# Kernel optimization log

Measured on AMD Instinct MI355X. Metric: run time of the kernel, lower is better.

The kernel has to match this reference:

```python
import jax, jax.numpy as jnp
import numpy as np

N_NODES = 50000
N_EDGES = 800000
NFEAT, NHID, NOUT = 128, 128, 64


def _glorot(key, shape):
    lim = 1.0 / np.sqrt(shape[0])
    return jax.random.uniform(key, shape, jnp.float32, -lim, lim)


def setup_inputs() -> dict:
    key = jax.random.key(0)
    ks = jax.random.split(key, 12)
    x = jax.random.normal(ks[0], (N_NODES, NFEAT), jnp.float32)
    edge_src = jax.random.randint(ks[1], (N_EDGES,), 0, N_NODES, jnp.int32)
    edge_dst = jax.random.randint(ks[2], (N_EDGES,), 0, N_NODES, jnp.int32)
    edge_w = jax.random.uniform(ks[3], (N_EDGES,), jnp.float32)  # normalized adj values
    # layer params: nfeat->nhid, nhid->nhid, nhid->nhid, nhid->nout
    W0, b0 = _glorot(ks[4], (NFEAT, NHID)), jnp.zeros((NHID,), jnp.float32)
    W1, b1 = _glorot(ks[5], (NHID, NHID)), jnp.zeros((NHID,), jnp.float32)
    W2, b2 = _glorot(ks[6], (NHID, NHID)), jnp.zeros((NHID,), jnp.float32)
    W3, b3 = _glorot(ks[7], (NHID, NOUT)), jnp.zeros((NOUT,), jnp.float32)
    return dict(x=x, edge_src=edge_src, edge_dst=edge_dst, edge_w=edge_w,
                W0=W0, b0=b0, W1=W1, b1=b1, W2=W2, b2=b2, W3=W3, b3=b3)


def _gcn_layer(h, src, dst, w, W, b):
    # support = h @ W ; out = A @ support + b  (A given as weighted edge list)
    support = h @ W                               # [N, d_out]
    msgs = support[src] * w[:, None]              # [E, d_out] gather + scale
    agg = jax.ops.segment_sum(msgs, dst, num_segments=N_NODES)  # scatter-add
    return agg + b


def reference(x, edge_src, edge_dst, edge_w, W0, b0, W1, b1, W2, b2, W3, b3):
    # eval mode: dropout is identity
    h = jax.nn.relu(_gcn_layer(x, edge_src, edge_dst, edge_w, W0, b0))
    h = jax.nn.relu(_gcn_layer(h, edge_src, edge_dst, edge_w, W1, b1))
    h = jax.nn.relu(_gcn_layer(h, edge_src, edge_dst, edge_w, W2, b2))
    h = _gcn_layer(h, edge_src, edge_dst, edge_w, W3, b3)  # no relu on last layer
    return h
```

## Files before the change

kernel.cpp:

```cpp
#include <hip/hip_runtime.h>


constexpr int NN = 50000;
constexpr int NE = 800000;
constexpr int NB = (NN + 127) >> 7;
constexpr int CAP = 4608;
constexpr int PART_CHUNK = 4096;
constexpr int PART_GRID = (NE + PART_CHUNK - 1) / PART_CHUNK;

typedef __attribute__((ext_vector_type(8))) short bf16x8;
typedef __attribute__((ext_vector_type(4))) float floatx4;
typedef __attribute__((ext_vector_type(2))) float floatx2;
typedef __attribute__((ext_vector_type(4))) unsigned int uintx4;
typedef __attribute__((ext_vector_type(2))) unsigned int uintx2;

__device__ inline unsigned short f2bf(float f) {
    unsigned u = __float_as_uint(f);
    u += 0x7fffu + ((u >> 16) & 1u);
    return (unsigned short)(u >> 16);
}
__device__ inline float bflo(unsigned v) { return __uint_as_float(v << 16); }
__device__ inline float bfhi(unsigned v) { return __uint_as_float(v & 0xffff0000u); }
__device__ inline unsigned char f2fp8(float f) {
    return (unsigned char)(__builtin_amdgcn_cvt_pk_fp8_f32(f, f, 0, false) & 0xff);
}


__global__ __launch_bounds__(256) void k_part(
        const int* __restrict__ src, const int* __restrict__ dst,
        const float* __restrict__ w, int* __restrict__ bfill,
        int2* __restrict__ ep) {
    __shared__ int hist[NB], base[NB], off[NB];
    int tid = threadIdx.x;
    for (int b = tid; b < NB; b += 256) { hist[b] = 0; off[b] = 0; }
    __syncthreads();

    int e0 = blockIdx.x * PART_CHUNK;
    int  sreg[16]; int wreg[16]; short breg[16];
#pragma unroll
    for (int i = 0; i < 16; ++i) {
        int e = e0 + i * 256 + tid;
        if (e < NE) {
            int d = dst[e];
            int b = d >> 7;
            sreg[i] = (src[e] & 0xffff) | ((d & 127) << 16);
            wreg[i] = __float_as_int(w[e]);
            breg[i] = (short)b;
            atomicAdd(&hist[b], 1);
        } else breg[i] = -1;
    }
    __syncthreads();
    for (int b = tid; b < NB; b += 256)
        base[b] = b * CAP + atomicAdd(&bfill[b], hist[b]);
    __syncthreads();
#pragma unroll
    for (int i = 0; i < 16; ++i) {
        if (breg[i] >= 0) {
            int b = breg[i];
            int p = atomicAdd(&off[b], 1);
            ep[base[b] + p] = make_int2(sreg[i], wreg[i]);
        }
    }
}

__global__ __launch_bounds__(256) void k_sort(
        const int2* __restrict__ ep, const int* __restrict__ bfill,
        unsigned* __restrict__ es, int2* __restrict__ begend) {
    __shared__ int cnt[128], base[128], fl[128];
    __shared__ int s_total;
    int b  = blockIdx.x;
    int n0 = b << 7;
    int nn = min(128, NN - n0);
    int t  = threadIdx.x;
    if (t < 128) { cnt[t] = 0; fl[t] = 0; }
    __syncthreads();
    int bbase = b * CAP;
    int beg = bbase, end = bbase + bfill[b];
    for (int e = beg + t; e < end; e += 256)
        atomicAdd(&cnt[(ep[e].x >> 16) & 127], 1);
    __syncthreads();
    int cp = (t < 128) ? ((cnt[t] + 3) & ~3) : 0;
    if (t < 128) base[t] = cp;
    __syncthreads();
    for (int off = 1; off < 128; off <<= 1) {
        int add = (t >= off && t < 128) ? base[t - off] : 0;
        __syncthreads();
        if (t < 128) base[t] += add;
        __syncthreads();
    }
    if (t == 127) s_total = base[127];
    __syncthreads();
    int total = s_total;
    for (int i = t; i < total + 16; i += 256) es[bbase + i] = 0u;
    if (t < nn) {
        int off = base[t] - cp;
        begend[n0 + t] = make_int2(bbase + off, bbase + off + cp);
    }
    __syncthreads();
    for (int e = beg + t; e < end; e += 256) {
        int2 v = ep[e];
        int d = (v.x >> 16) & 127;
        int off = base[d] - ((cnt[d] + 3) & ~3);
        int pos = bbase + off + atomicAdd(&fl[d], 1);
        es[pos] = (unsigned)(v.x & 0xffff) |
                  ((unsigned)f2bf(__int_as_float(v.y)) << 16);
    }
}


__global__ void k_prep(
        const float* __restrict__ W0, const float* __restrict__ W1,
        const float* __restrict__ W2, const float* __restrict__ W3,
        unsigned short* __restrict__ T0, unsigned short* __restrict__ T1,
        unsigned short* __restrict__ T2, unsigned short* __restrict__ T3,
        int* __restrict__ bfill) {
    int b = blockIdx.x;
    if (b == 448) {
        for (int i = threadIdx.x; i < NB; i += 128) bfill[i] = 0;
        return;
    }
    const float* W; unsigned short* T; int N, n;
    if (b < 128)      { W = W0; T = T0; N = 128; n = b; }
    else if (b < 256) { W = W1; T = T1; N = 128; n = b - 128; }
    else if (b < 384) { W = W2; T = T2; N = 128; n = b - 256; }
    else              { W = W3; T = T3; N = 64;  n = b - 384; }
    int k = threadIdx.x;
    T[n * 128 + k] = f2bf(W[(size_t)k * N + n]);
}


__device__ inline bf16x8 ldA_f32(const float* A, size_t off) {
    float4 u = *(const float4*)&A[off];
    float4 v = *(const float4*)&A[off + 4];
    bf16x8 r;
    r[0] = (short)f2bf(u.x); r[1] = (short)f2bf(u.y);
    r[2] = (short)f2bf(u.z); r[3] = (short)f2bf(u.w);
    r[4] = (short)f2bf(v.x); r[5] = (short)f2bf(v.y);
    r[6] = (short)f2bf(v.z); r[7] = (short)f2bf(v.w);
    return r;
}

__global__ __launch_bounds__(256) void k_gemm0(
        const float* __restrict__ A,
        const unsigned short* __restrict__ Wt,
        unsigned char* __restrict__ C,
        int M) {
    constexpr int STR = 136;
    __shared__ unsigned short sWt[128 * STR];

    const int tid = threadIdx.x;
#pragma unroll
    for (int i = 0; i < 8; ++i) {
        int c = i * 256 + tid;
        int row = c >> 4, col = (c & 15) * 8;
        *(uint4*)&sWt[row * STR + col] = *(const uint4*)&Wt[row * 128 + col];
    }

    const int wv = tid >> 6;
    const int ln = tid & 63;
    const int m  = ln & 15;
    const int qd = ln >> 4;

    int gr  = blockIdx.x * 64 + wv * 16 + m;
    int grc = (gr < M) ? gr : (M - 1);
    bf16x8 af[4];
#pragma unroll
    for (int s = 0; s < 4; ++s)
        af[s] = ldA_f32(A, (size_t)grc * 128 + s * 32 + qd * 8);

    __syncthreads();

    floatx4 acc[8];
#pragma unroll
    for (int c = 0; c < 8; ++c) {
        acc[c] = (floatx4){0.f, 0.f, 0.f, 0.f};
#pragma unroll
        for (int s = 0; s < 4; ++s) {
            bf16x8 bf = *(const bf16x8*)&sWt[(c * 16 + m) * STR + s * 32 + qd * 8];
            acc[c] = __builtin_amdgcn_mfma_f32_16x16x32_bf16(af[s], bf, acc[c], 0, 0, 0);
        }
    }

    int row0 = blockIdx.x * 64 + wv * 16 + qd * 4;
#pragma unroll
    for (int c = 0; c < 8; ++c)
#pragma unroll
        for (int r = 0; r < 4; ++r) {
            int row = row0 + r;
            if (row < M) {
                int col = c * 16 + m;
                int sl  = col >> 6;
                C[(size_t)sl * NN * 64 + (size_t)row * 64 + (col & 63)] =
                    f2fp8(acc[c][r]);
            }
        }
}


template<int NO, typename CT>
__global__ __launch_bounds__(256) void k_gemmh(
        const unsigned short* __restrict__ A,
        const unsigned short* __restrict__ Wt,
        CT* __restrict__ C,
        int M) {
    constexpr int STR = 136;
    __shared__ unsigned short sWt[NO * STR];

    const int tid = threadIdx.x;
#pragma unroll
    for (int i = 0; i < NO / 16; ++i) {
        int c = i * 256 + tid;
        int row = c >> 4, col = (c & 15) * 8;
        *(uint4*)&sWt[row * STR + col] = *(const uint4*)&Wt[row * 128 + col];
    }

    const int wv = tid >> 6;
    const int ln = tid & 63;
    const int m  = ln & 15;
    const int qd = ln >> 4;

    int gr  = blockIdx.x * 64 + wv * 16 + m;
    int grc = (gr < M) ? gr : (M - 1);
    bf16x8 af[4];
#pragma unroll
    for (int s = 0; s < 4; ++s)
        af[s] = __builtin_nontemporal_load(
            (const bf16x8*)&A[(size_t)grc * 128 + s * 32 + qd * 8]);

    __syncthreads();

    floatx4 acc[NO / 16];
#pragma unroll
    for (int c = 0; c < NO / 16; ++c) {
        acc[c] = (floatx4){0.f, 0.f, 0.f, 0.f};
#pragma unroll
        for (int s = 0; s < 4; ++s) {
            bf16x8 bf = *(const bf16x8*)&sWt[(c * 16 + m) * STR + s * 32 + qd * 8];
            acc[c] = __builtin_amdgcn_mfma_f32_16x16x32_bf16(af[s], bf, acc[c], 0, 0, 0);
        }
    }

    int row0 = blockIdx.x * 64 + wv * 16 + qd * 4;
#pragma unroll
    for (int c = 0; c < NO / 16; ++c)
#pragma unroll
        for (int r = 0; r < 4; ++r) {
            int row = row0 + r;
            if (row < M) {
                int col = c * 16 + m;
                if constexpr (sizeof(CT) == 1) {
                    int sl = col >> 6;
                    C[(size_t)sl * NN * 64 + (size_t)row * 64 + (col & 63)] =
                        (CT)f2fp8(acc[c][r]);
                } else {
                    int sl = col >> 5;
                    C[(size_t)sl * NN * 32 + (size_t)row * 32 + (col & 31)] =
                        (CT)f2bf(acc[c][r]);
                }
            }
        }
}


#define FMAP8(W, R)                                                             \
    { floatx2 p0 = __builtin_amdgcn_cvt_pk_f32_fp8((int)(R).x, false);          \
      floatx2 p1 = __builtin_amdgcn_cvt_pk_f32_fp8((int)(R).x, true);           \
      floatx2 p2 = __builtin_amdgcn_cvt_pk_f32_fp8((int)(R).y, false);          \
      floatx2 p3 = __builtin_amdgcn_cvt_pk_f32_fp8((int)(R).y, true);           \
      acc[0] = fmaf(W, p0.x, acc[0]); acc[1] = fmaf(W, p0.y, acc[1]);           \
      acc[2] = fmaf(W, p1.x, acc[2]); acc[3] = fmaf(W, p1.y, acc[3]);           \
      acc[4] = fmaf(W, p2.x, acc[4]); acc[5] = fmaf(W, p2.y, acc[5]);           \
      acc[6] = fmaf(W, p3.x, acc[6]); acc[7] = fmaf(W, p3.y, acc[7]); }

__global__ __launch_bounds__(256, 8) void k_aggh(
        const unsigned char* __restrict__ sup,
        const int2* __restrict__ begend, const unsigned* __restrict__ es,
        const float* __restrict__ bias,
        unsigned short* __restrict__ h) {
    const int bid  = blockIdx.x;
    const int sl   = bid & 1;
    const int tile = bid >> 1;
    const int tid  = threadIdx.x;
    const int l    = tid & 7;
    const int n    = tile * 32 + (tid >> 3);
    const bool nv  = n < NN;
    const unsigned char* supS = sup + (size_t)sl * NN * 64;
    const float* biasS = bias + sl * 64;

    int2 be = nv ? begend[n] : make_int2(0, 0);
    const int e0 = be.x, en = be.y;
    int e = e0;
    float acc[8] = {0.f, 0.f, 0.f, 0.f, 0.f, 0.f, 0.f, 0.f};
    bool v = e < en;
    if (__any(v)) {
        uintx4 mv = __builtin_nontemporal_load((const uintx4*)&es[e0]);
        for (;;) {
            uint2 r0 = *(const uint2*)&supS[(size_t)(mv[0] & 0xffffu) * 64 + l * 8];
            uint2 r1 = *(const uint2*)&supS[(size_t)(mv[1] & 0xffffu) * 64 + l * 8];
            uint2 r2 = *(const uint2*)&supS[(size_t)(mv[2] & 0xffffu) * 64 + l * 8];
            uint2 r3 = *(const uint2*)&supS[(size_t)(mv[3] & 0xffffu) * 64 + l * 8];
            float w0 = v ? bfhi(mv[0]) : 0.f;
            float w1 = v ? bfhi(mv[1]) : 0.f;
            float w2 = v ? bfhi(mv[2]) : 0.f;
            float w3 = v ? bfhi(mv[3]) : 0.f;
            e += 4;
            v = e < en;
            bool more = __any(v);
            int eo = v ? e : e0;
            uintx4 mn = __builtin_nontemporal_load((const uintx4*)&es[eo]);
            FMAP8(w0, r0); FMAP8(w1, r1); FMAP8(w2, r2); FMAP8(w3, r3);
            mv = mn;
            if (!more) break;
        }
    }
    if (nv) {
        uintx4 pk;
#pragma unroll
        for (int q = 0; q < 4; ++q) {
            float a0 = fmaxf(acc[2 * q]     + biasS[l * 8 + 2 * q],     0.f);
            float a1 = fmaxf(acc[2 * q + 1] + biasS[l * 8 + 2 * q + 1], 0.f);
            pk[q] = (unsigned)f2bf(a0) | ((unsigned)f2bf(a1) << 16);
        }
        __builtin_nontemporal_store(
            pk, (uintx4*)&h[(size_t)n * 128 + sl * 64 + l * 8]);
    }
}


#define FMA4(W, R)                                                              \
    acc[0] = fmaf(W, bflo((R).x), acc[0]); acc[1] = fmaf(W, bfhi((R).x), acc[1]); \
    acc[2] = fmaf(W, bflo((R).y), acc[2]); acc[3] = fmaf(W, bfhi((R).y), acc[3]);

__global__ __launch_bounds__(256, 8) void k_aggo(
        const unsigned short* __restrict__ sup,
        const int2* __restrict__ begend, const unsigned* __restrict__ es,
        const float* __restrict__ bias, float* __restrict__ out) {
    const int bid  = blockIdx.x;
    const int sl   = bid & 1;
    const int tile = bid >> 1;
    const int tid  = threadIdx.x;
    const int l    = tid & 7;
    const int n    = tile * 32 + (tid >> 3);
    const bool nv  = n < NN;
    const unsigned short* supS = sup + (size_t)sl * NN * 32;
    const float* biasS = bias + sl * 32;

    int2 be = nv ? begend[n] : make_int2(0, 0);
    const int e0 = be.x, en = be.y;
    int e = e0;
    float acc[4] = {0.f, 0.f, 0.f, 0.f};
    bool v = e < en;
    if (__any(v)) {
        uintx4 mv = __builtin_nontemporal_load((const uintx4*)&es[e0]);
        for (;;) {
            uint2 r0 = *(const uint2*)&supS[(size_t)(mv[0] & 0xffffu) * 32 + l * 4];
            uint2 r1 = *(const uint2*)&supS[(size_t)(mv[1] & 0xffffu) * 32 + l * 4];
            uint2 r2 = *(const uint2*)&supS[(size_t)(mv[2] & 0xffffu) * 32 + l * 4];
            uint2 r3 = *(const uint2*)&supS[(size_t)(mv[3] & 0xffffu) * 32 + l * 4];
            float w0 = v ? bfhi(mv[0]) : 0.f;
            float w1 = v ? bfhi(mv[1]) : 0.f;
            float w2 = v ? bfhi(mv[2]) : 0.f;
            float w3 = v ? bfhi(mv[3]) : 0.f;
            e += 4;
            v = e < en;
            bool more = __any(v);
            int eo = v ? e : e0;
            uintx4 mn = __builtin_nontemporal_load((const uintx4*)&es[eo]);
            FMA4(w0, r0); FMA4(w1, r1); FMA4(w2, r2); FMA4(w3, r3);
            mv = mn;
            if (!more) break;
        }
    }
    if (nv) {
        float4 o = make_float4(acc[0] + biasS[l * 4],
                               acc[1] + biasS[l * 4 + 1],
                               acc[2] + biasS[l * 4 + 2],
                               acc[3] + biasS[l * 4 + 3]);
        *(float4*)&out[(size_t)n * 64 + sl * 32 + l * 4] = o;
    }
}


extern "C" void kernel_launch(void* const* d_in, const int* in_sizes, int n_in,
                              void* d_out, int out_size, void* d_ws, size_t ws_size,
                              hipStream_t stream) {
    (void)in_sizes; (void)n_in; (void)out_size; (void)ws_size;

    const float* x    = (const float*)d_in[0];
    const int*   esrc = (const int*)d_in[1];
    const int*   edst = (const int*)d_in[2];
    const float* ew   = (const float*)d_in[3];
    const float* W0   = (const float*)d_in[4];
    const float* b0   = (const float*)d_in[5];
    const float* W1   = (const float*)d_in[6];
    const float* b1   = (const float*)d_in[7];
    const float* W2   = (const float*)d_in[8];
    const float* b2   = (const float*)d_in[9];
    const float* W3   = (const float*)d_in[10];
    const float* b3   = (const float*)d_in[11];

    char* p = (char*)d_ws;
    auto alloc = [&](size_t bytes) {
        char* r = p;
        p += (bytes + 511) & ~size_t(511);
        return r;
    };
    int*      bfill  = (int*)     alloc((size_t)NB * 4);
    int2*     begend = (int2*)    alloc((size_t)NN * 8);
    int2*     ep     = (int2*)    alloc((size_t)NB * CAP * 8);
    unsigned* es     = (unsigned*)alloc((size_t)NB * CAP * 4);
    unsigned char*  s8a  = (unsigned char*) alloc((size_t)NN * 128);
    unsigned char*  s8b  = (unsigned char*) alloc((size_t)NN * 128);
    unsigned short* s16  = (unsigned short*)alloc((size_t)NN * 64 * 2);
    unsigned short* hbuf = (unsigned short*)alloc((size_t)NN * 128 * 2);
    unsigned short* Wt0 = (unsigned short*)alloc((size_t)128 * 128 * 2);
    unsigned short* Wt1 = (unsigned short*)alloc((size_t)128 * 128 * 2);
    unsigned short* Wt2 = (unsigned short*)alloc((size_t)128 * 128 * 2);
    unsigned short* Wt3 = (unsigned short*)alloc((size_t)64 * 128 * 2);

    k_prep<<<449, 128, 0, stream>>>(W0, W1, W2, W3, Wt0, Wt1, Wt2, Wt3, bfill);
    k_part<<<PART_GRID, 256, 0, stream>>>(esrc, edst, ew, bfill, ep);
    k_sort<<<NB, 256, 0, stream>>>(ep, bfill, es, begend);

    const int g_gemm = (NN + 63) / 64;
    const int g_agg  = ((NN + 31) / 32) * 2;

    k_gemm0<<<g_gemm, 256, 0, stream>>>(x, Wt0, s8a, NN);
    k_aggh<<<g_agg, 256, 0, stream>>>(s8a, begend, es, b0, hbuf);
    k_gemmh<128, unsigned char><<<g_gemm, 256, 0, stream>>>(hbuf, Wt1, s8b, NN);
    k_aggh<<<g_agg, 256, 0, stream>>>(s8b, begend, es, b1, hbuf);
    k_gemmh<128, unsigned char><<<g_gemm, 256, 0, stream>>>(hbuf, Wt2, s8a, NN);
    k_aggh<<<g_agg, 256, 0, stream>>>(s8a, begend, es, b2, hbuf);
    k_gemmh<64, unsigned short><<<g_gemm, 256, 0, stream>>>(hbuf, Wt3, s16, NN);
    k_aggo<<<g_agg, 256, 0, stream>>>(s16, begend, es, b3, (float*)d_out);
}
```

Baseline: 253.3 us.

## Build CSR with global per-node histogram, scan, and atomic scatter; unroll aggregation by eight

Replaces the two-pass bucketed partition and sort with a per-node histogram, a block scan that claims segments from a global cursor, and a direct atomic scatter into a compact CSR edge array. Each node's segment is padded to a multiple of eight, and the aggregation kernels now load eight edges per iteration instead of four, so more gather loads are in flight. In exchange the build uses global atomics on 50k counters and a scatter whose order within a segment is nondeterministic. Padding to eight also adds more zero-weight padding entries that the aggregation still reads.

```diff
diff --git a/kernel.cpp b/kernel.cpp
--- a/kernel.cpp
+++ b/kernel.cpp
@@ -4,15 +4,12 @@
 constexpr int NN = 50000;
 constexpr int NE = 800000;
 constexpr int NB = (NN + 127) >> 7;
-constexpr int CAP = 4608;
-constexpr int PART_CHUNK = 4096;
-constexpr int PART_GRID = (NE + PART_CHUNK - 1) / PART_CHUNK;
+constexpr int ES_CAP = NE + 7 * NN + 64;
 
 typedef __attribute__((ext_vector_type(8))) short bf16x8;
 typedef __attribute__((ext_vector_type(4))) float floatx4;
 typedef __attribute__((ext_vector_type(2))) float floatx2;
 typedef __attribute__((ext_vector_type(4))) unsigned int uintx4;
-typedef __attribute__((ext_vector_type(2))) unsigned int uintx2;
 
 __device__ inline unsigned short f2bf(float f) {
     unsigned u = __float_as_uint(f);
@@ -26,84 +23,68 @@
 }
 
 
-__global__ __launch_bounds__(256) void k_part(
-        const int* __restrict__ src, const int* __restrict__ dst,
-        const float* __restrict__ w, int* __restrict__ bfill,
-        int2* __restrict__ ep) {
-    __shared__ int hist[NB], base[NB], off[NB];
-    int tid = threadIdx.x;
-    for (int b = tid; b < NB; b += 256) { hist[b] = 0; off[b] = 0; }
-    __syncthreads();
-
-    int e0 = blockIdx.x * PART_CHUNK;
-    int  sreg[16]; int wreg[16]; short breg[16];
-#pragma unroll
-    for (int i = 0; i < 16; ++i) {
-        int e = e0 + i * 256 + tid;
-        if (e < NE) {
-            int d = dst[e];
-            int b = d >> 7;
-            sreg[i] = (src[e] & 0xffff) | ((d & 127) << 16);
-            wreg[i] = __float_as_int(w[e]);
-            breg[i] = (short)b;
-            atomicAdd(&hist[b], 1);
-        } else breg[i] = -1;
-    }
-    __syncthreads();
-    for (int b = tid; b < NB; b += 256)
-        base[b] = b * CAP + atomicAdd(&bfill[b], hist[b]);
-    __syncthreads();
-#pragma unroll
-    for (int i = 0; i < 16; ++i) {
-        if (breg[i] >= 0) {
-            int b = breg[i];
-            int p = atomicAdd(&off[b], 1);
-            ep[base[b] + p] = make_int2(sreg[i], wreg[i]);
-        }
-    }
-}
-
-__global__ __launch_bounds__(256) void k_sort(
-        const int2* __restrict__ ep, const int* __restrict__ bfill,
-        unsigned* __restrict__ es, int2* __restrict__ begend) {
-    __shared__ int cnt[128], base[128], fl[128];
-    __shared__ int s_total;
-    int b  = blockIdx.x;
-    int n0 = b << 7;
-    int nn = min(128, NN - n0);
-    int t  = threadIdx.x;
-    if (t < 128) { cnt[t] = 0; fl[t] = 0; }
-    __syncthreads();
-    int bbase = b * CAP;
-    int beg = bbase, end = bbase + bfill[b];
-    for (int e = beg + t; e < end; e += 256)
-        atomicAdd(&cnt[(ep[e].x >> 16) & 127], 1);
-    __syncthreads();
-    int cp = (t < 128) ? ((cnt[t] + 3) & ~3) : 0;
-    if (t < 128) base[t] = cp;
+__global__ __launch_bounds__(256) void k_hist(
+        const int* __restrict__ dst, int* __restrict__ cnt) {
+    int i = blockIdx.x * 1024 + threadIdx.x * 4;
+    if (i + 3 < NE) {
+        int4 d = *(const int4*)&dst[i];
+        atomicAdd(&cnt[d.x], 1); atomicAdd(&cnt[d.y], 1);
+        atomicAdd(&cnt[d.z], 1); atomicAdd(&cnt[d.w], 1);
+    } else {
+        for (int e = i; e < NE; ++e) atomicAdd(&cnt[dst[e]], 1);
+    }
+}
+
+__global__ __launch_bounds__(128) void k_scan(
+        const int* __restrict__ cnt, int* __restrict__ cursor,
+        int2* __restrict__ begend, unsigned* __restrict__ es) {
+    __shared__ int s[128];
+    __shared__ int soff;
+    int t = threadIdx.x;
+    int n = blockIdx.x * 128 + t;
+    int c = (n < NN) ? cnt[n] : 0;
+    int p8 = (c + 7) & ~7;
+    s[t] = p8;
     __syncthreads();
     for (int off = 1; off < 128; off <<= 1) {
-        int add = (t >= off && t < 128) ? base[t - off] : 0;
+        int add = (t >= off) ? s[t - off] : 0;
         __syncthreads();
-        if (t < 128) base[t] += add;
+        s[t] += add;
         __syncthreads();
     }
-    if (t == 127) s_total = base[127];
+    if (t == 127) soff = atomicAdd(cursor, s[127]);
+    int incl = s[t];
     __syncthreads();
-    int total = s_total;
-    for (int i = t; i < total + 16; i += 256) es[bbase + i] = 0u;
-    if (t < nn) {
-        int off = base[t] - cp;
-        begend[n0 + t] = make_int2(bbase + off, bbase + off + cp);
-    }
-    __syncthreads();
-    for (int e = beg + t; e < end; e += 256) {
-        int2 v = ep[e];
-        int d = (v.x >> 16) & 127;
-        int off = base[d] - ((cnt[d] + 3) & ~3);
-        int pos = bbase + off + atomicAdd(&fl[d], 1);
-        es[pos] = (unsigned)(v.x & 0xffff) |
-                  ((unsigned)f2bf(__int_as_float(v.y)) << 16);
+    int beg = soff + incl - p8;
+    if (n < NN) {
+        begend[n] = make_int2(beg, beg + c);
+        for (int i = c; i < p8; ++i) es[beg + i] = 0u;
+    }
+}
+
+__global__ __launch_bounds__(256) void k_scatter(
+        const int* __restrict__ src, const int* __restrict__ dst,
+        const float* __restrict__ w, const int2* __restrict__ begend,
+        int* __restrict__ fill, unsigned* __restrict__ es) {
+    int i = blockIdx.x * 1024 + threadIdx.x * 4;
+    if (i + 3 < NE) {
+        int4 s = *(const int4*)&src[i];
+        int4 d = *(const int4*)&dst[i];
+        float4 ww = *(const float4*)&w[i];
+        int p0 = begend[d.x].x + atomicAdd(&fill[d.x], 1);
+        es[p0] = (unsigned)(s.x & 0xffff) | ((unsigned)f2bf(ww.x) << 16);
+        int p1 = begend[d.y].x + atomicAdd(&fill[d.y], 1);
+        es[p1] = (unsigned)(s.y & 0xffff) | ((unsigned)f2bf(ww.y) << 16);
+        int p2 = begend[d.z].x + atomicAdd(&fill[d.z], 1);
+        es[p2] = (unsigned)(s.z & 0xffff) | ((unsigned)f2bf(ww.z) << 16);
+        int p3 = begend[d.w].x + atomicAdd(&fill[d.w], 1);
+        es[p3] = (unsigned)(s.w & 0xffff) | ((unsigned)f2bf(ww.w) << 16);
+    } else {
+        for (int e = i; e < NE; ++e) {
+            int d = dst[e];
+            int p = begend[d].x + atomicAdd(&fill[d], 1);
+            es[p] = (unsigned)(src[e] & 0xffff) | ((unsigned)f2bf(w[e]) << 16);
+        }
     }
 }
 
@@ -113,10 +94,14 @@
         const float* __restrict__ W2, const float* __restrict__ W3,
         unsigned short* __restrict__ T0, unsigned short* __restrict__ T1,
         unsigned short* __restrict__ T2, unsigned short* __restrict__ T3,
-        int* __restrict__ bfill) {
+        int* __restrict__ cnt, int* __restrict__ fill, int* __restrict__ cursor) {
     int b = blockIdx.x;
-    if (b == 448) {
-        for (int i = threadIdx.x; i < NB; i += 128) bfill[i] = 0;
+    if (b >= 448) {
+        int q = b - 448;
+        for (int i = q * 128 + threadIdx.x; i < NN; i += 16 * 128) {
+            cnt[i] = 0; fill[i] = 0;
+        }
+        if (b == 448 && threadIdx.x == 0) *cursor = 0;
         return;
     }
     const float* W; unsigned short* T; int N, n;
@@ -293,23 +278,34 @@
     float acc[8] = {0.f, 0.f, 0.f, 0.f, 0.f, 0.f, 0.f, 0.f};
     bool v = e < en;
     if (__any(v)) {
-        uintx4 mv = __builtin_nontemporal_load((const uintx4*)&es[e0]);
+        uintx4 m0 = __builtin_nontemporal_load((const uintx4*)&es[e0]);
+        uintx4 m1 = __builtin_nontemporal_load((const uintx4*)&es[e0 + 4]);
         for (;;) {
-            uint2 r0 = *(const uint2*)&supS[(size_t)(mv[0] & 0xffffu) * 64 + l * 8];
-            uint2 r1 = *(const uint2*)&supS[(size_t)(mv[1] & 0xffffu) * 64 + l * 8];
-            uint2 r2 = *(const uint2*)&supS[(size_t)(mv[2] & 0xffffu) * 64 + l * 8];
-            uint2 r3 = *(const uint2*)&supS[(size_t)(mv[3] & 0xffffu) * 64 + l * 8];
-            float w0 = v ? bfhi(mv[0]) : 0.f;
-            float w1 = v ? bfhi(mv[1]) : 0.f;
-            float w2 = v ? bfhi(mv[2]) : 0.f;
-            float w3 = v ? bfhi(mv[3]) : 0.f;
-            e += 4;
+            uint2 r0 = *(const uint2*)&supS[(size_t)(m0[0] & 0xffffu) * 64 + l * 8];
+            uint2 r1 = *(const uint2*)&supS[(size_t)(m0[1] & 0xffffu) * 64 + l * 8];
+            uint2 r2 = *(const uint2*)&supS[(size_t)(m0[2] & 0xffffu) * 64 + l * 8];
+            uint2 r3 = *(const uint2*)&supS[(size_t)(m0[3] & 0xffffu) * 64 + l * 8];
+            uint2 r4 = *(const uint2*)&supS[(size_t)(m1[0] & 0xffffu) * 64 + l * 8];
+            uint2 r5 = *(const uint2*)&supS[(size_t)(m1[1] & 0xffffu) * 64 + l * 8];
+            uint2 r6 = *(const uint2*)&supS[(size_t)(m1[2] & 0xffffu) * 64 + l * 8];
+            uint2 r7 = *(const uint2*)&supS[(size_t)(m1[3] & 0xffffu) * 64 + l * 8];
+            float w0 = v ? bfhi(m0[0]) : 0.f;
+            float w1 = v ? bfhi(m0[1]) : 0.f;
+            float w2 = v ? bfhi(m0[2]) : 0.f;
+            float w3 = v ? bfhi(m0[3]) : 0.f;
+            float w4 = v ? bfhi(m1[0]) : 0.f;
+            float w5 = v ? bfhi(m1[1]) : 0.f;
+            float w6 = v ? bfhi(m1[2]) : 0.f;
+            float w7 = v ? bfhi(m1[3]) : 0.f;
+            e += 8;
             v = e < en;
             bool more = __any(v);
             int eo = v ? e : e0;
-            uintx4 mn = __builtin_nontemporal_load((const uintx4*)&es[eo]);
+            uintx4 n0 = __builtin_nontemporal_load((const uintx4*)&es[eo]);
+            uintx4 n1 = __builtin_nontemporal_load((const uintx4*)&es[eo + 4]);
             FMAP8(w0, r0); FMAP8(w1, r1); FMAP8(w2, r2); FMAP8(w3, r3);
-            mv = mn;
+            FMAP8(w4, r4); FMAP8(w5, r5); FMAP8(w6, r6); FMAP8(w7, r7);
+            m0 = n0; m1 = n1;
             if (!more) break;
         }
     }
@@ -351,23 +347,34 @@
     float acc[4] = {0.f, 0.f, 0.f, 0.f};
     bool v = e < en;
     if (__any(v)) {
-        uintx4 mv = __builtin_nontemporal_load((const uintx4*)&es[e0]);
+        uintx4 m0 = __builtin_nontemporal_load((const uintx4*)&es[e0]);
+        uintx4 m1 = __builtin_nontemporal_load((const uintx4*)&es[e0 + 4]);
         for (;;) {
-            uint2 r0 = *(const uint2*)&supS[(size_t)(mv[0] & 0xffffu) * 32 + l * 4];
-            uint2 r1 = *(const uint2*)&supS[(size_t)(mv[1] & 0xffffu) * 32 + l * 4];
-            uint2 r2 = *(const uint2*)&supS[(size_t)(mv[2] & 0xffffu) * 32 + l * 4];
-            uint2 r3 = *(const uint2*)&supS[(size_t)(mv[3] & 0xffffu) * 32 + l * 4];
-            float w0 = v ? bfhi(mv[0]) : 0.f;
-            float w1 = v ? bfhi(mv[1]) : 0.f;
-            float w2 = v ? bfhi(mv[2]) : 0.f;
-            float w3 = v ? bfhi(mv[3]) : 0.f;
-            e += 4;
+            uint2 r0 = *(const uint2*)&supS[(size_t)(m0[0] & 0xffffu) * 32 + l * 4];
+            uint2 r1 = *(const uint2*)&supS[(size_t)(m0[1] & 0xffffu) * 32 + l * 4];
+            uint2 r2 = *(const uint2*)&supS[(size_t)(m0[2] & 0xffffu) * 32 + l * 4];
+            uint2 r3 = *(const uint2*)&supS[(size_t)(m0[3] & 0xffffu) * 32 + l * 4];
+            uint2 r4 = *(const uint2*)&supS[(size_t)(m1[0] & 0xffffu) * 32 + l * 4];
+            uint2 r5 = *(const uint2*)&supS[(size_t)(m1[1] & 0xffffu) * 32 + l * 4];
+            uint2 r6 = *(const uint2*)&supS[(size_t)(m1[2] & 0xffffu) * 32 + l * 4];
+            uint2 r7 = *(const uint2*)&supS[(size_t)(m1[3] & 0xffffu) * 32 + l * 4];
+            float w0 = v ? bfhi(m0[0]) : 0.f;
+            float w1 = v ? bfhi(m0[1]) : 0.f;
+            float w2 = v ? bfhi(m0[2]) : 0.f;
+            float w3 = v ? bfhi(m0[3]) : 0.f;
+            float w4 = v ? bfhi(m1[0]) : 0.f;
+            float w5 = v ? bfhi(m1[1]) : 0.f;
+            float w6 = v ? bfhi(m1[2]) : 0.f;
+            float w7 = v ? bfhi(m1[3]) : 0.f;
+            e += 8;
             v = e < en;
             bool more = __any(v);
             int eo = v ? e : e0;
-            uintx4 mn = __builtin_nontemporal_load((const uintx4*)&es[eo]);
+            uintx4 n0 = __builtin_nontemporal_load((const uintx4*)&es[eo]);
+            uintx4 n1 = __builtin_nontemporal_load((const uintx4*)&es[eo + 4]);
             FMA4(w0, r0); FMA4(w1, r1); FMA4(w2, r2); FMA4(w3, r3);
-            mv = mn;
+            FMA4(w4, r4); FMA4(w5, r5); FMA4(w6, r6); FMA4(w7, r7);
+            m0 = n0; m1 = n1;
             if (!more) break;
         }
     }
@@ -405,10 +412,11 @@
         p += (bytes + 511) & ~size_t(511);
         return r;
     };
-    int*      bfill  = (int*)     alloc((size_t)NB * 4);
+    int*      cnt    = (int*)     alloc((size_t)NN * 4);
+    int*      fill   = (int*)     alloc((size_t)NN * 4);
+    int*      cursor = (int*)     alloc(64);
     int2*     begend = (int2*)    alloc((size_t)NN * 8);
-    int2*     ep     = (int2*)    alloc((size_t)NB * CAP * 8);
-    unsigned* es     = (unsigned*)alloc((size_t)NB * CAP * 4);
+    unsigned* es     = (unsigned*)alloc((size_t)ES_CAP * 4);
     unsigned char*  s8a  = (unsigned char*) alloc((size_t)NN * 128);
     unsigned char*  s8b  = (unsigned char*) alloc((size_t)NN * 128);
     unsigned short* s16  = (unsigned short*)alloc((size_t)NN * 64 * 2);
@@ -418,12 +426,15 @@
     unsigned short* Wt2 = (unsigned short*)alloc((size_t)128 * 128 * 2);
     unsigned short* Wt3 = (unsigned short*)alloc((size_t)64 * 128 * 2);
 
-    k_prep<<<449, 128, 0, stream>>>(W0, W1, W2, W3, Wt0, Wt1, Wt2, Wt3, bfill);
-    k_part<<<PART_GRID, 256, 0, stream>>>(esrc, edst, ew, bfill, ep);
-    k_sort<<<NB, 256, 0, stream>>>(ep, bfill, es, begend);
-
+    const int g_edge = (NE + 1023) / 1024;
     const int g_gemm = (NN + 63) / 64;
     const int g_agg  = ((NN + 31) / 32) * 2;
+
+    k_prep<<<464, 128, 0, stream>>>(W0, W1, W2, W3, Wt0, Wt1, Wt2, Wt3,
+                                    cnt, fill, cursor);
+    k_hist<<<g_edge, 256, 0, stream>>>(edst, cnt);
+    k_scan<<<NB, 128, 0, stream>>>(cnt, cursor, begend, es);
+    k_scatter<<<g_edge, 256, 0, stream>>>(esrc, edst, ew, begend, fill, es);
 
     k_gemm0<<<g_gemm, 256, 0, stream>>>(x, Wt0, s8a, NN);
     k_aggh<<<g_agg, 256, 0, stream>>>(s8a, begend, es, b0, hbuf);
```

Result: slower. 317.6 us (+25.4%).

## Pad edge segments to 16 and unroll aggregation gathers by sixteen

Applied to the files above, without the earlier changes.

Per-node edge segments in the sorted edge list are now padded to multiples of 16 instead of 4. Both aggregation kernels process 16 edges per iteration, issuing 16 independent row gathers before the FMAs, and prefetch the next 16 edge records. Finished lanes read a dedicated zeroed region, which removes the per-lane weight masking. The aim is more memory-level parallelism on the latency-bound gathers, at the cost of extra zero-weight padding gathers, higher register pressure (launch bounds lowered from 8 to 6 waves), and more of the fixed edge buffer used by padding.

```diff
diff --git a/kernel.cpp b/kernel.cpp
--- a/kernel.cpp
+++ b/kernel.cpp
@@ -7,12 +7,12 @@
 constexpr int CAP = 4608;
 constexpr int PART_CHUNK = 4096;
 constexpr int PART_GRID = (NE + PART_CHUNK - 1) / PART_CHUNK;
+constexpr int ZOFF = NB * CAP;
 
 typedef __attribute__((ext_vector_type(8))) short bf16x8;
 typedef __attribute__((ext_vector_type(4))) float floatx4;
 typedef __attribute__((ext_vector_type(2))) float floatx2;
 typedef __attribute__((ext_vector_type(4))) unsigned int uintx4;
-typedef __attribute__((ext_vector_type(2))) unsigned int uintx2;
 
 __device__ inline unsigned short f2bf(float f) {
     unsigned u = __float_as_uint(f);
@@ -79,7 +79,7 @@
     for (int e = beg + t; e < end; e += 256)
         atomicAdd(&cnt[(ep[e].x >> 16) & 127], 1);
     __syncthreads();
-    int cp = (t < 128) ? ((cnt[t] + 3) & ~3) : 0;
+    int cp = (t < 128) ? ((cnt[t] + 15) & ~15) : 0;
     if (t < 128) base[t] = cp;
     __syncthreads();
     for (int off = 1; off < 128; off <<= 1) {
@@ -100,7 +100,7 @@
     for (int e = beg + t; e < end; e += 256) {
         int2 v = ep[e];
         int d = (v.x >> 16) & 127;
-        int off = base[d] - ((cnt[d] + 3) & ~3);
+        int off = base[d] - ((cnt[d] + 15) & ~15);
         int pos = bbase + off + atomicAdd(&fl[d], 1);
         es[pos] = (unsigned)(v.x & 0xffff) |
                   ((unsigned)f2bf(__int_as_float(v.y)) << 16);
@@ -113,10 +113,11 @@
         const float* __restrict__ W2, const float* __restrict__ W3,
         unsigned short* __restrict__ T0, unsigned short* __restrict__ T1,
         unsigned short* __restrict__ T2, unsigned short* __restrict__ T3,
-        int* __restrict__ bfill) {
+        int* __restrict__ bfill, unsigned* __restrict__ es) {
     int b = blockIdx.x;
     if (b == 448) {
         for (int i = threadIdx.x; i < NB; i += 128) bfill[i] = 0;
+        if (threadIdx.x < 16) es[ZOFF + threadIdx.x] = 0u;
         return;
     }
     const float* W; unsigned short* T; int N, n;
@@ -272,7 +273,10 @@
       acc[4] = fmaf(W, p2.x, acc[4]); acc[5] = fmaf(W, p2.y, acc[5]);           \
       acc[6] = fmaf(W, p3.x, acc[6]); acc[7] = fmaf(W, p3.y, acc[7]); }
 
-__global__ __launch_bounds__(256, 8) void k_aggh(
+#define GATH8(R, MV)                                                            \
+    uint2 R = *(const uint2*)&supS[(size_t)((MV) & 0xffffu) * 64 + l * 8];
+
+__global__ __launch_bounds__(256, 6) void k_aggh(
         const unsigned char* __restrict__ sup,
         const int2* __restrict__ begend, const unsigned* __restrict__ es,
         const float* __restrict__ bias,
@@ -293,23 +297,33 @@
     float acc[8] = {0.f, 0.f, 0.f, 0.f, 0.f, 0.f, 0.f, 0.f};
     bool v = e < en;
     if (__any(v)) {
-        uintx4 mv = __builtin_nontemporal_load((const uintx4*)&es[e0]);
+        int ei = v ? e0 : ZOFF;
+        uintx4 m0 = __builtin_nontemporal_load((const uintx4*)&es[ei]);
+        uintx4 m1 = __builtin_nontemporal_load((const uintx4*)&es[ei + 4]);
+        uintx4 m2 = __builtin_nontemporal_load((const uintx4*)&es[ei + 8]);
+        uintx4 m3 = __builtin_nontemporal_load((const uintx4*)&es[ei + 12]);
         for (;;) {
-            uint2 r0 = *(const uint2*)&supS[(size_t)(mv[0] & 0xffffu) * 64 + l * 8];
-            uint2 r1 = *(const uint2*)&supS[(size_t)(mv[1] & 0xffffu) * 64 + l * 8];
-            uint2 r2 = *(const uint2*)&supS[(size_t)(mv[2] & 0xffffu) * 64 + l * 8];
-            uint2 r3 = *(const uint2*)&supS[(size_t)(mv[3] & 0xffffu) * 64 + l * 8];
-            float w0 = v ? bfhi(mv[0]) : 0.f;
-            float w1 = v ? bfhi(mv[1]) : 0.f;
-            float w2 = v ? bfhi(mv[2]) : 0.f;
-            float w3 = v ? bfhi(mv[3]) : 0.f;
-            e += 4;
+            GATH8(r0, m0[0]); GATH8(r1, m0[1]); GATH8(r2, m0[2]); GATH8(r3, m0[3]);
+            GATH8(r4, m1[0]); GATH8(r5, m1[1]); GATH8(r6, m1[2]); GATH8(r7, m1[3]);
+            GATH8(r8, m2[0]); GATH8(r9, m2[1]); GATH8(ra, m2[2]); GATH8(rb, m2[3]);
+            GATH8(rc, m3[0]); GATH8(rd, m3[1]); GATH8(re, m3[2]); GATH8(rf, m3[3]);
+            float w0 = bfhi(m0[0]), w1 = bfhi(m0[1]), w2 = bfhi(m0[2]), w3 = bfhi(m0[3]);
+            float w4 = bfhi(m1[0]), w5 = bfhi(m1[1]), w6 = bfhi(m1[2]), w7 = bfhi(m1[3]);
+            float w8 = bfhi(m2[0]), w9 = bfhi(m2[1]), wa = bfhi(m2[2]), wb = bfhi(m2[3]);
+            float wc = bfhi(m3[0]), wd = bfhi(m3[1]), we = bfhi(m3[2]), wf = bfhi(m3[3]);
+            e += 16;
             v = e < en;
             bool more = __any(v);
-            int eo = v ? e : e0;
-            uintx4 mn = __builtin_nontemporal_load((const uintx4*)&es[eo]);
+            int eo = v ? e : ZOFF;
+            uintx4 n0 = __builtin_nontemporal_load((const uintx4*)&es[eo]);
+            uintx4 n1 = __builtin_nontemporal_load((const uintx4*)&es[eo + 4]);
+            uintx4 n2 = __builtin_nontemporal_load((const uintx4*)&es[eo + 8]);
+            uintx4 n3 = __builtin_nontemporal_load((const uintx4*)&es[eo + 12]);
             FMAP8(w0, r0); FMAP8(w1, r1); FMAP8(w2, r2); FMAP8(w3, r3);
-            mv = mn;
+            FMAP8(w4, r4); FMAP8(w5, r5); FMAP8(w6, r6); FMAP8(w7, r7);
+            FMAP8(w8, r8); FMAP8(w9, r9); FMAP8(wa, ra); FMAP8(wb, rb);
+            FMAP8(wc, rc); FMAP8(wd, rd); FMAP8(we, re); FMAP8(wf, rf);
+            m0 = n0; m1 = n1; m2 = n2; m3 = n3;
             if (!more) break;
         }
     }
@@ -331,7 +345,10 @@
     acc[0] = fmaf(W, bflo((R).x), acc[0]); acc[1] = fmaf(W, bfhi((R).x), acc[1]); \
     acc[2] = fmaf(W, bflo((R).y), acc[2]); acc[3] = fmaf(W, bfhi((R).y), acc[3]);
 
-__global__ __launch_bounds__(256, 8) void k_aggo(
+#define GATH4(R, MV)                                                            \
+    uint2 R = *(const uint2*)&supS[(size_t)((MV) & 0xffffu) * 32 + l * 4];
+
+__global__ __launch_bounds__(256, 6) void k_aggo(
         const unsigned short* __restrict__ sup,
         const int2* __restrict__ begend, const unsigned* __restrict__ es,
         const float* __restrict__ bias, float* __restrict__ out) {
@@ -351,23 +368,33 @@
     float acc[4] = {0.f, 0.f, 0.f, 0.f};
     bool v = e < en;
     if (__any(v)) {
-        uintx4 mv = __builtin_nontemporal_load((const uintx4*)&es[e0]);
+        int ei = v ? e0 : ZOFF;
+        uintx4 m0 = __builtin_nontemporal_load((const uintx4*)&es[ei]);
+        uintx4 m1 = __builtin_nontemporal_load((const uintx4*)&es[ei + 4]);
+        uintx4 m2 = __builtin_nontemporal_load((const uintx4*)&es[ei + 8]);
+        uintx4 m3 = __builtin_nontemporal_load((const uintx4*)&es[ei + 12]);
         for (;;) {
-            uint2 r0 = *(const uint2*)&supS[(size_t)(mv[0] & 0xffffu) * 32 + l * 4];
-            uint2 r1 = *(const uint2*)&supS[(size_t)(mv[1] & 0xffffu) * 32 + l * 4];
-            uint2 r2 = *(const uint2*)&supS[(size_t)(mv[2] & 0xffffu) * 32 + l * 4];
-            uint2 r3 = *(const uint2*)&supS[(size_t)(mv[3] & 0xffffu) * 32 + l * 4];
-            float w0 = v ? bfhi(mv[0]) : 0.f;
-            float w1 = v ? bfhi(mv[1]) : 0.f;
-            float w2 = v ? bfhi(mv[2]) : 0.f;
-            float w3 = v ? bfhi(mv[3]) : 0.f;
-            e += 4;
+            GATH4(r0, m0[0]); GATH4(r1, m0[1]); GATH4(r2, m0[2]); GATH4(r3, m0[3]);
+            GATH4(r4, m1[0]); GATH4(r5, m1[1]); GATH4(r6, m1[2]); GATH4(r7, m1[3]);
+            GATH4(r8, m2[0]); GATH4(r9, m2[1]); GATH4(ra, m2[2]); GATH4(rb, m2[3]);
+            GATH4(rc, m3[0]); GATH4(rd, m3[1]); GATH4(re, m3[2]); GATH4(rf, m3[3]);
+            float w0 = bfhi(m0[0]), w1 = bfhi(m0[1]), w2 = bfhi(m0[2]), w3 = bfhi(m0[3]);
+            float w4 = bfhi(m1[0]), w5 = bfhi(m1[1]), w6 = bfhi(m1[2]), w7 = bfhi(m1[3]);
+            float w8 = bfhi(m2[0]), w9 = bfhi(m2[1]), wa = bfhi(m2[2]), wb = bfhi(m2[3]);
+            float wc = bfhi(m3[0]), wd = bfhi(m3[1]), we = bfhi(m3[2]), wf = bfhi(m3[3]);
+            e += 16;
             v = e < en;
             bool more = __any(v);
-            int eo = v ? e : e0;
-            uintx4 mn = __builtin_nontemporal_load((const uintx4*)&es[eo]);
+            int eo = v ? e : ZOFF;
+            uintx4 n0 = __builtin_nontemporal_load((const uintx4*)&es[eo]);
+            uintx4 n1 = __builtin_nontemporal_load((const uintx4*)&es[eo + 4]);
+            uintx4 n2 = __builtin_nontemporal_load((const uintx4*)&es[eo + 8]);
+            uintx4 n3 = __builtin_nontemporal_load((const uintx4*)&es[eo + 12]);
             FMA4(w0, r0); FMA4(w1, r1); FMA4(w2, r2); FMA4(w3, r3);
-            mv = mn;
+            FMA4(w4, r4); FMA4(w5, r5); FMA4(w6, r6); FMA4(w7, r7);
+            FMA4(w8, r8); FMA4(w9, r9); FMA4(wa, ra); FMA4(wb, rb);
+            FMA4(wc, rc); FMA4(wd, rd); FMA4(we, re); FMA4(wf, rf);
+            m0 = n0; m1 = n1; m2 = n2; m3 = n3;
             if (!more) break;
         }
     }
@@ -408,7 +435,7 @@
     int*      bfill  = (int*)     alloc((size_t)NB * 4);
     int2*     begend = (int2*)    alloc((size_t)NN * 8);
     int2*     ep     = (int2*)    alloc((size_t)NB * CAP * 8);
-    unsigned* es     = (unsigned*)alloc((size_t)NB * CAP * 4);
+    unsigned* es     = (unsigned*)alloc(((size_t)NB * CAP + 64) * 4);
     unsigned char*  s8a  = (unsigned char*) alloc((size_t)NN * 128);
     unsigned char*  s8b  = (unsigned char*) alloc((size_t)NN * 128);
     unsigned short* s16  = (unsigned short*)alloc((size_t)NN * 64 * 2);
@@ -418,7 +445,8 @@
     unsigned short* Wt2 = (unsigned short*)alloc((size_t)128 * 128 * 2);
     unsigned short* Wt3 = (unsigned short*)alloc((size_t)64 * 128 * 2);
 
-    k_prep<<<449, 128, 0, stream>>>(W0, W1, W2, W3, Wt0, Wt1, Wt2, Wt3, bfill);
+    k_prep<<<449, 128, 0, stream>>>(W0, W1, W2, W3, Wt0, Wt1, Wt2, Wt3,
+                                    bfill, es);
     k_part<<<PART_GRID, 256, 0, stream>>>(esrc, edst, ew, bfill, ep);
     k_sort<<<NB, 256, 0, stream>>>(ep, bfill, es, begend);
 
```

After: 249.2 us. Within noise of the previous version (-1.6%).
